# Optimization experiments

Hardware: AMD Instinct MI355X
Metric: run time of the kernel (lower is better)

The kernel has to match this reference:

```python
import jax, jax.numpy as jnp
import numpy as np

N, T, I, H = 16, 4096, 256, 512

def setup_inputs() -> dict:
    key = jax.random.key(0)
    k1, k2, k3, k4, k5 = jax.random.split(key, 5)
    x = jax.random.normal(k1, (N, T, I), dtype=jnp.float32)
    initial = jax.random.normal(k2, (N, H), dtype=jnp.float32)
    # nn.Linear params: y = x @ W.T + b
    Wi = jax.random.normal(k3, (H, I), dtype=jnp.float32) * (1.0 / np.sqrt(I))
    bi = jax.random.normal(k4, (H,), dtype=jnp.float32) * 0.01
    Whh = jax.random.normal(k5, (H, H), dtype=jnp.float32) * (1.0 / np.sqrt(H))
    return {"x": x, "initial": initial, "Wi": Wi, "bi": bi, "Whh": Whh}

def reference(x, initial, Wi, bi, Whh):
    # Precompute input projection for all timesteps: [N, T, H]
    proj = jnp.einsum('nti,hi->nth', x, Wi) + bi
    # h_0 = initial + Wi x[:,0]; h_t = Whh h_{t-1} + Wi x[:,t-1] for t >= 1
    h0 = initial + proj[:, 0]
    # inputs to scan: proj[:, 0:T-1] as [T-1, N, H] (note x[:,t-1] indexing)
    scan_in = jnp.swapaxes(proj[:, :T - 1], 0, 1)

    def step(h, p):
        h_new = h @ Whh.T + p
        return h_new, h_new

    _, ys = jax.lax.scan(step, h0, scan_in)  # ys: [T-1, N, H]
    hiddens = jnp.concatenate([h0[None], ys], axis=0)  # [T, N, H]
    hidden_tensor = jnp.swapaxes(hiddens, 0, 1)  # [N, T, H]
    return (hidden_tensor, hidden_tensor)
```

## Files before the change

kernel.cpp:

```cpp
#include <hip/hip_runtime.h>


constexpr int NN = 16;
constexpr int TT = 4096;
constexpr int II = 256;
constexpr int HH = 512;
constexpr int CK = 16;
constexpr int NC = 256;
constexpr long NTH = (long)NN * TT * HH;
constexpr int NMATS = 11;

__device__ __forceinline__ float4 ld4(const float* p) { return *(const float4*)p; }

#define FMA16(W_, e0, e1, e2, e3) \
    acc0.x = fmaf(e0, (W_).x, acc0.x); acc0.y = fmaf(e0, (W_).y, acc0.y); \
    acc0.z = fmaf(e0, (W_).z, acc0.z); acc0.w = fmaf(e0, (W_).w, acc0.w); \
    acc1.x = fmaf(e1, (W_).x, acc1.x); acc1.y = fmaf(e1, (W_).y, acc1.y); \
    acc1.z = fmaf(e1, (W_).z, acc1.z); acc1.w = fmaf(e1, (W_).w, acc1.w); \
    acc2.x = fmaf(e2, (W_).x, acc2.x); acc2.y = fmaf(e2, (W_).y, acc2.y); \
    acc2.z = fmaf(e2, (W_).z, acc2.z); acc2.w = fmaf(e2, (W_).w, acc2.w); \
    acc3.x = fmaf(e3, (W_).x, acc3.x); acc3.y = fmaf(e3, (W_).y, acc3.y); \
    acc3.z = fmaf(e3, (W_).z, acc3.z); acc3.w = fmaf(e3, (W_).w, acc3.w);

#define COMPUTE(sl) \
    FMA16(wv##sl[0], hv##sl[0].x, hv##sl[1].x, hv##sl[2].x, hv##sl[3].x) \
    FMA16(wv##sl[1], hv##sl[0].y, hv##sl[1].y, hv##sl[2].y, hv##sl[3].y) \
    FMA16(wv##sl[2], hv##sl[0].z, hv##sl[1].z, hv##sl[2].z, hv##sl[3].z) \
    FMA16(wv##sl[3], hv##sl[0].w, hv##sl[1].w, hv##sl[2].w, hv##sl[3].w)

#define PRE_PH(sl, kk) { \
    const float* wp_ = WT + (size_t)(4 * (kk)) * HH + j; \
    wv##sl[0] = ld4(wp_);            wv##sl[1] = ld4(wp_ + HH); \
    wv##sl[2] = ld4(wp_ + 2 * HH);   wv##sl[3] = ld4(wp_ + 3 * HH); \
    hv##sl[0] = hs[hb0 + (((kk)) ^ sw0)]; hv##sl[1] = hs[hb1 + (((kk)) ^ sw0)]; \
    hv##sl[2] = hs[hb2 + (((kk)) ^ sw1)]; hv##sl[3] = hs[hb3 + (((kk)) ^ sw1)]; }

#define PIPE_DECL float4 wv0[4], wv1[4], wv2[4], wv3[4]; \
                  float4 hv0[4], hv1[4], hv2[4], hv3[4];

__global__ __launch_bounds__(256) void trg_kernel(
    const float* __restrict__ src, float* __restrict__ dst, int R, int C)
{
    __shared__ float tile[32][33];
    const size_t mo = (size_t)blockIdx.z * R * C;
    const int x0 = blockIdx.x * 32, y0 = blockIdx.y * 32;
    const int tx = threadIdx.x & 31, ty = threadIdx.x >> 5;
#pragma unroll
    for (int r = 0; r < 4; r++)
        tile[ty + 8 * r][tx] = src[mo + (size_t)(y0 + ty + 8 * r) * C + (x0 + tx)];
    __syncthreads();
#pragma unroll
    for (int r = 0; r < 4; r++)
        dst[mo + (size_t)(x0 + ty + 8 * r) * R + (y0 + tx)] = tile[tx][ty + 8 * r];
}

__global__ __launch_bounds__(256) void proj_kernel(
    const float* __restrict__ x, const float* __restrict__ WiT,
    const float* __restrict__ bi, float* __restrict__ Bh)
{
    const int t0 = blockIdx.x * 32;
    const int j0 = blockIdx.y * 128;
    const int n  = blockIdx.z;
    __shared__ float4 xs[32 * 64];

    {
        const int r  = threadIdx.x >> 3;
        const int ci = threadIdx.x & 7;
        int s = t0 + r - 1; if (s < 0) s = 0;
        const float4* src = (const float4*)(x + ((size_t)n * TT + s) * II);
        const int rb = r * 64, rs = r >> 2;
#pragma unroll
        for (int q = 0; q < 8; q++) xs[rb + ((ci + 8 * q) ^ rs)] = src[ci + 8 * q];
    }
    __syncthreads();

    const int tj  = threadIdx.x & 31;
    const int tt4 = threadIdx.x >> 5;
    const int j   = j0 + tj * 4;
    const int xb0 = (tt4 * 4 + 0) * 64, xb1 = (tt4 * 4 + 1) * 64;
    const int xb2 = (tt4 * 4 + 2) * 64, xb3 = (tt4 * 4 + 3) * 64;
    const int swx = tt4;

    float4 acc0 = {0,0,0,0}, acc1 = {0,0,0,0}, acc2 = {0,0,0,0}, acc3 = {0,0,0,0};
    PIPE_DECL
#define PRE_PJ(sl, kk) { \
    const float* wp_ = WiT + (size_t)(4 * (kk)) * HH + j; \
    wv##sl[0] = ld4(wp_);            wv##sl[1] = ld4(wp_ + HH); \
    wv##sl[2] = ld4(wp_ + 2 * HH);   wv##sl[3] = ld4(wp_ + 3 * HH); \
    hv##sl[0] = xs[xb0 + (((kk)) ^ swx)]; hv##sl[1] = xs[xb1 + (((kk)) ^ swx)]; \
    hv##sl[2] = xs[xb2 + (((kk)) ^ swx)]; hv##sl[3] = xs[xb3 + (((kk)) ^ swx)]; }

    PRE_PJ(0, 0) PRE_PJ(1, 1) PRE_PJ(2, 2) PRE_PJ(3, 3)
    for (int g = 0; g < 15; g++) {
        const int kq = g * 4;
        COMPUTE(0) PRE_PJ(0, kq + 4)
        COMPUTE(1) PRE_PJ(1, kq + 5)
        COMPUTE(2) PRE_PJ(2, kq + 6)
        COMPUTE(3) PRE_PJ(3, kq + 7)
    }
    COMPUTE(0) COMPUTE(1) COMPUTE(2) COMPUTE(3)

    const float4 bv = ld4(bi + j);
    {
        const int tb = t0 + tt4 * 4;
        *(float4*)(Bh + ((size_t)n * TT + tb + 0) * HH + j) =
            make_float4(acc0.x + bv.x, acc0.y + bv.y, acc0.z + bv.z, acc0.w + bv.w);
        *(float4*)(Bh + ((size_t)n * TT + tb + 1) * HH + j) =
            make_float4(acc1.x + bv.x, acc1.y + bv.y, acc1.z + bv.z, acc1.w + bv.w);
        *(float4*)(Bh + ((size_t)n * TT + tb + 2) * HH + j) =
            make_float4(acc2.x + bv.x, acc2.y + bv.y, acc2.z + bv.z, acc2.w + bv.w);
        *(float4*)(Bh + ((size_t)n * TT + tb + 3) * HH + j) =
            make_float4(acc3.x + bv.x, acc3.y + bv.y, acc3.z + bv.z, acc3.w + bv.w);
    }
}

template <int PHASE>
__global__ __launch_bounds__(512, 2) void phase_kernel(
    const float* __restrict__ WT,
    float* __restrict__ Bh,
    const float* __restrict__ init_,
    const float* __restrict__ Gin,
    float* __restrict__ Zout,
    float* __restrict__ outA)
{
    __shared__ float4 hs[NN * 128];
    const int c   = blockIdx.x;
    const int tid = threadIdx.x;
    const int nq  = tid & 3;
    const int n0  = nq * 4;
    const int jq  = tid >> 2;
    const int j   = jq * 4;
    const int hb0 = (n0 + 0) * 128, hb1 = (n0 + 1) * 128;
    const int hb2 = (n0 + 2) * 128, hb3 = (n0 + 3) * 128;
    const int sw0 = nq * 2, sw1 = nq * 2 + 1;

    {
        float4 v[4];
        if (c == 0) {
#pragma unroll
            for (int rr = 0; rr < 4; rr++) {
                const int nn = n0 + rr;
                float4 iv = ld4(init_ + (size_t)nn * HH + j);
                float4 bv = ld4(Bh + (size_t)nn * TT * HH + j);
                v[rr] = make_float4(iv.x + bv.x, iv.y + bv.y, iv.z + bv.z, iv.w + bv.w);
                if (PHASE == 3) {
                    *(float4*)(outA + (size_t)nn * TT * HH + j) = v[rr];
                    *(float4*)(Bh   + (size_t)nn * TT * HH + j) = v[rr];
                }
            }
        } else if (PHASE == 1) {
            const int t0 = c * CK;
#pragma unroll
            for (int rr = 0; rr < 4; rr++)
                v[rr] = ld4(Bh + ((size_t)(n0 + rr) * TT + t0) * HH + j);
        } else {
#pragma unroll
            for (int rr = 0; rr < 4; rr++)
                v[rr] = ld4(Gin + (size_t)(c - 1) * NN * HH + (size_t)(n0 + rr) * HH + j);
        }
        hs[hb0 + (jq ^ sw0)] = v[0];
        hs[hb1 + (jq ^ sw0)] = v[1];
        hs[hb2 + (jq ^ sw1)] = v[2];
        hs[hb3 + (jq ^ sw1)] = v[3];
    }
    __syncthreads();

    const int tstart = (PHASE == 1) ? (c * CK + 1) : ((c == 0) ? 1 : c * CK);
    const int tend   = c * CK + CK;

    for (int t = tstart; t < tend; t++) {
        float* bp0 = Bh + ((size_t)(n0 + 0) * TT + t) * HH + j;
        float* bp1 = Bh + ((size_t)(n0 + 1) * TT + t) * HH + j;
        float* bp2 = Bh + ((size_t)(n0 + 2) * TT + t) * HH + j;
        float* bp3 = Bh + ((size_t)(n0 + 3) * TT + t) * HH + j;
        float4 b0 = ld4(bp0), b1 = ld4(bp1), b2 = ld4(bp2), b3 = ld4(bp3);

        float4 acc0 = {0,0,0,0}, acc1 = {0,0,0,0}, acc2 = {0,0,0,0}, acc3 = {0,0,0,0};
        PIPE_DECL
        PRE_PH(0, 0) PRE_PH(1, 1) PRE_PH(2, 2) PRE_PH(3, 3)
        for (int g = 0; g < 31; g++) {
            const int kq = g * 4;
            COMPUTE(0) PRE_PH(0, kq + 4)
            COMPUTE(1) PRE_PH(1, kq + 5)
            COMPUTE(2) PRE_PH(2, kq + 6)
            COMPUTE(3) PRE_PH(3, kq + 7)
        }
        COMPUTE(0) COMPUTE(1) COMPUTE(2) COMPUTE(3)

        float4 o0 = make_float4(acc0.x + b0.x, acc0.y + b0.y, acc0.z + b0.z, acc0.w + b0.w);
        float4 o1 = make_float4(acc1.x + b1.x, acc1.y + b1.y, acc1.z + b1.z, acc1.w + b1.w);
        float4 o2 = make_float4(acc2.x + b2.x, acc2.y + b2.y, acc2.z + b2.z, acc2.w + b2.w);
        float4 o3 = make_float4(acc3.x + b3.x, acc3.y + b3.y, acc3.z + b3.z, acc3.w + b3.w);

        __syncthreads();
        hs[hb0 + (jq ^ sw0)] = o0;
        hs[hb1 + (jq ^ sw0)] = o1;
        hs[hb2 + (jq ^ sw1)] = o2;
        hs[hb3 + (jq ^ sw1)] = o3;
        if (PHASE == 3) {
            *(float4*)(outA + ((size_t)(n0 + 0) * TT + t) * HH + j) = o0;
            *(float4*)(outA + ((size_t)(n0 + 1) * TT + t) * HH + j) = o1;
            *(float4*)(outA + ((size_t)(n0 + 2) * TT + t) * HH + j) = o2;
            *(float4*)(outA + ((size_t)(n0 + 3) * TT + t) * HH + j) = o3;
            *(float4*)bp0 = o0; *(float4*)bp1 = o1;
            *(float4*)bp2 = o2; *(float4*)bp3 = o3;
        }
        __syncthreads();
    }

    if (PHASE == 1) {
        float* zp = Zout + (size_t)c * NN * HH;
        *(float4*)(zp + (size_t)(n0 + 0) * HH + j) = hs[hb0 + (jq ^ sw0)];
        *(float4*)(zp + (size_t)(n0 + 1) * HH + j) = hs[hb1 + (jq ^ sw0)];
        *(float4*)(zp + (size_t)(n0 + 2) * HH + j) = hs[hb2 + (jq ^ sw1)];
        *(float4*)(zp + (size_t)(n0 + 3) * HH + j) = hs[hb3 + (jq ^ sw1)];
    }
}

__global__ __launch_bounds__(256) void sq_kernel(
    const float* __restrict__ A, float* __restrict__ Out)
{
    const int j0 = blockIdx.x * 128;
    const int a0 = blockIdx.y * 16;
    __shared__ float4 As[16 * 128];
    {
#pragma unroll
        for (int rr = 0; rr < 8; rr++) {
            int idx = threadIdx.x + rr * 256;
            int row = idx >> 7, s = idx & 127;
            As[row * 128 + (s ^ (row >> 2))] = ld4(A + (size_t)(a0 + row) * HH + s * 4);
        }
    }
    __syncthreads();

    const int jh = threadIdx.x & 63;
    const int j  = j0 + jh * 2;
    const int rq = threadIdx.x >> 6;
    const int ab0 = (rq * 4 + 0) * 128, ab1 = (rq * 4 + 1) * 128;
    const int ab2 = (rq * 4 + 2) * 128, ab3 = (rq * 4 + 3) * 128;

    float2 bw0[4], bw1[4], bw2[4], bw3[4];
    float4 av0[4], av1[4], av2[4], av3[4];
    float2 c0 = {0,0}, c1 = {0,0}, c2 = {0,0}, c3 = {0,0};
#define SQ_PRE(sl, kk) { \
    const float* bp_ = A + (size_t)(4 * (kk)) * HH + j; \
    bw##sl[0] = *(const float2*)(bp_);            bw##sl[1] = *(const float2*)(bp_ + HH); \
    bw##sl[2] = *(const float2*)(bp_ + 2 * HH);   bw##sl[3] = *(const float2*)(bp_ + 3 * HH); \
    av##sl[0] = As[ab0 + (((kk)) ^ rq)]; av##sl[1] = As[ab1 + (((kk)) ^ rq)]; \
    av##sl[2] = As[ab2 + (((kk)) ^ rq)]; av##sl[3] = As[ab3 + (((kk)) ^ rq)]; }
#define SQ_F(Bv_, e0, e1, e2, e3) \
    c0.x = fmaf(e0, (Bv_).x, c0.x); c0.y = fmaf(e0, (Bv_).y, c0.y); \
    c1.x = fmaf(e1, (Bv_).x, c1.x); c1.y = fmaf(e1, (Bv_).y, c1.y); \
    c2.x = fmaf(e2, (Bv_).x, c2.x); c2.y = fmaf(e2, (Bv_).y, c2.y); \
    c3.x = fmaf(e3, (Bv_).x, c3.x); c3.y = fmaf(e3, (Bv_).y, c3.y);
#define SQ_C(sl) \
    SQ_F(bw##sl[0], av##sl[0].x, av##sl[1].x, av##sl[2].x, av##sl[3].x) \
    SQ_F(bw##sl[1], av##sl[0].y, av##sl[1].y, av##sl[2].y, av##sl[3].y) \
    SQ_F(bw##sl[2], av##sl[0].z, av##sl[1].z, av##sl[2].z, av##sl[3].z) \
    SQ_F(bw##sl[3], av##sl[0].w, av##sl[1].w, av##sl[2].w, av##sl[3].w)

    SQ_PRE(0, 0) SQ_PRE(1, 1) SQ_PRE(2, 2) SQ_PRE(3, 3)
    for (int g = 0; g < 31; g++) {
        const int kq = g * 4;
        SQ_C(0) SQ_PRE(0, kq + 4)
        SQ_C(1) SQ_PRE(1, kq + 5)
        SQ_C(2) SQ_PRE(2, kq + 6)
        SQ_C(3) SQ_PRE(3, kq + 7)
    }
    SQ_C(0) SQ_C(1) SQ_C(2) SQ_C(3)

    *(float2*)(Out + (size_t)(a0 + rq * 4 + 0) * HH + j) = c0;
    *(float2*)(Out + (size_t)(a0 + rq * 4 + 1) * HH + j) = c1;
    *(float2*)(Out + (size_t)(a0 + rq * 4 + 2) * HH + j) = c2;
    *(float2*)(Out + (size_t)(a0 + rq * 4 + 3) * HH + j) = c3;
}

__global__ __launch_bounds__(512, 2) void ks_kernel(
    const float* __restrict__ Gin, float* __restrict__ Gout,
    const float* __restrict__ WT, int sft)
{
    __shared__ float4 hs[NN * 128];
    const int c   = blockIdx.x;
    const int tid = threadIdx.x;

    if (c < sft) {
        const float4* src = (const float4*)(Gin + (size_t)c * NN * HH);
        float4* dst = (float4*)(Gout + (size_t)c * NN * HH);
#pragma unroll
        for (int r = 0; r < 4; r++) dst[tid + r * 512] = src[tid + r * 512];
        return;
    }

    const int nq  = tid & 3;
    const int n0  = nq * 4;
    const int jq  = tid >> 2;
    const int j   = jq * 4;
    const int hb0 = (n0 + 0) * 128, hb1 = (n0 + 1) * 128;
    const int hb2 = (n0 + 2) * 128, hb3 = (n0 + 3) * 128;
    const int sw0 = nq * 2, sw1 = nq * 2 + 1;

    float4 g[4];
    {
        const float* sp = Gin + (size_t)(c - sft) * NN * HH;
        const float* gp = Gin + (size_t)c * NN * HH;
        float4 v[4];
#pragma unroll
        for (int rr = 0; rr < 4; rr++) {
            v[rr] = ld4(sp + (size_t)(n0 + rr) * HH + j);
            g[rr] = ld4(gp + (size_t)(n0 + rr) * HH + j);
        }
        hs[hb0 + (jq ^ sw0)] = v[0];
        hs[hb1 + (jq ^ sw0)] = v[1];
        hs[hb2 + (jq ^ sw1)] = v[2];
        hs[hb3 + (jq ^ sw1)] = v[3];
    }
    __syncthreads();

    float4 acc0 = {0,0,0,0}, acc1 = {0,0,0,0}, acc2 = {0,0,0,0}, acc3 = {0,0,0,0};
    PIPE_DECL
    PRE_PH(0, 0) PRE_PH(1, 1) PRE_PH(2, 2) PRE_PH(3, 3)
    for (int g2 = 0; g2 < 31; g2++) {
        const int kq = g2 * 4;
        COMPUTE(0) PRE_PH(0, kq + 4)
        COMPUTE(1) PRE_PH(1, kq + 5)
        COMPUTE(2) PRE_PH(2, kq + 6)
        COMPUTE(3) PRE_PH(3, kq + 7)
    }
    COMPUTE(0) COMPUTE(1) COMPUTE(2) COMPUTE(3)

    float* op = Gout + (size_t)c * NN * HH;
    *(float4*)(op + (size_t)(n0 + 0) * HH + j) =
        make_float4(g[0].x + acc0.x, g[0].y + acc0.y, g[0].z + acc0.z, g[0].w + acc0.w);
    *(float4*)(op + (size_t)(n0 + 1) * HH + j) =
        make_float4(g[1].x + acc1.x, g[1].y + acc1.y, g[1].z + acc1.z, g[1].w + acc1.w);
    *(float4*)(op + (size_t)(n0 + 2) * HH + j) =
        make_float4(g[2].x + acc2.x, g[2].y + acc2.y, g[2].z + acc2.z, g[2].w + acc2.w);
    *(float4*)(op + (size_t)(n0 + 3) * HH + j) =
        make_float4(g[3].x + acc3.x, g[3].y + acc3.y, g[3].z + acc3.z, g[3].w + acc3.w);
}

extern "C" void kernel_launch(void* const* d_in, const int* in_sizes, int n_in,
                              void* d_out, int out_size, void* d_ws, size_t ws_size,
                              hipStream_t stream)
{
    const float* x    = (const float*)d_in[0];
    const float* ini  = (const float*)d_in[1];
    const float* Wi   = (const float*)d_in[2];
    const float* bi   = (const float*)d_in[3];
    const float* Whh  = (const float*)d_in[4];
    float* out   = (float*)d_out;
    float* halfB = out + NTH;
    float* mats  = out + NTH - (long)NMATS * HH * HH;
    float* matsT = out + NTH - (long)(NMATS + 8) * HH * HH;
    float* WiT   = matsT - (long)II * HH;
    float* G0 = (float*)d_ws;
    float* G1 = G0 + (size_t)NC * NN * HH;

    trg_kernel<<<dim3(II / 32, HH / 32, 1), 256, 0, stream>>>(Wi, WiT, HH, II);
    proj_kernel<<<dim3(TT / 32, HH / 128, NN), 256, 0, stream>>>(x, WiT, bi, halfB);

    trg_kernel<<<dim3(16, 16, 1), 256, 0, stream>>>(Whh, G1, HH, HH);

    phase_kernel<1><<<dim3(NC), 512, 0, stream>>>(G1, halfB, ini, nullptr, G0, nullptr);

    sq_kernel<<<dim3(4, 32), 256, 0, stream>>>(Whh, mats);
    for (int i = 1; i < NMATS; i++)
        sq_kernel<<<dim3(4, 32), 256, 0, stream>>>(mats + (size_t)(i - 1) * HH * HH,
                                                   mats + (size_t)i * HH * HH);
    trg_kernel<<<dim3(16, 16, 8), 256, 0, stream>>>(mats + (size_t)3 * HH * HH, matsT,
                                                    HH, HH);

    for (int r = 0; r < 8; r++) {
        const float* src = (r & 1) ? G1 : G0;
        float* dst       = (r & 1) ? G0 : G1;
        ks_kernel<<<dim3(NC), 512, 0, stream>>>(src, dst,
                                                matsT + (size_t)r * HH * HH, 1 << r);
    }

    trg_kernel<<<dim3(16, 16, 1), 256, 0, stream>>>(Whh, G1, HH, HH);

    phase_kernel<3><<<dim3(NC), 512, 0, stream>>>(G1, halfB, ini, G0, nullptr, out);
}
```

Before: 2.129 ms.

## Halve chunk length to 512 chunks, add scan round, hoist weight preloads

Halves the chunk length to 8 timesteps and doubles the chunk count to 512. This shortens the serial per-chunk recurrence in both phase kernels, at the cost of one extra Kogge-Stone round using an additional matrix power. The first W prefetch moves out of the timestep loop and is re-issued at the tail of each step, and per-step pointer recomputation becomes pointer increments. Buffers are re-laid out: the carry buffer lives partly in the output tail, and the transposed Whh is computed once and reused instead of being transposed twice.

```diff
diff --git a/kernel.cpp b/kernel.cpp
--- a/kernel.cpp
+++ b/kernel.cpp
@@ -5,10 +5,11 @@
 constexpr int TT = 4096;
 constexpr int II = 256;
 constexpr int HH = 512;
-constexpr int CK = 16;
-constexpr int NC = 256;
+constexpr int CK = 8;
+constexpr int NC = 512;
 constexpr long NTH = (long)NN * TT * HH;
 constexpr int NMATS = 11;
+constexpr int NKS = 9;
 
 __device__ __forceinline__ float4 ld4(const float* p) { return *(const float4*)p; }
 
@@ -28,12 +29,14 @@
     FMA16(wv##sl[2], hv##sl[0].z, hv##sl[1].z, hv##sl[2].z, hv##sl[3].z) \
     FMA16(wv##sl[3], hv##sl[0].w, hv##sl[1].w, hv##sl[2].w, hv##sl[3].w)
 
-#define PRE_PH(sl, kk) { \
+#define PRE_W(sl, kk) { \
     const float* wp_ = WT + (size_t)(4 * (kk)) * HH + j; \
     wv##sl[0] = ld4(wp_);            wv##sl[1] = ld4(wp_ + HH); \
-    wv##sl[2] = ld4(wp_ + 2 * HH);   wv##sl[3] = ld4(wp_ + 3 * HH); \
+    wv##sl[2] = ld4(wp_ + 2 * HH);   wv##sl[3] = ld4(wp_ + 3 * HH); }
+#define PRE_H(sl, kk) { \
     hv##sl[0] = hs[hb0 + (((kk)) ^ sw0)]; hv##sl[1] = hs[hb1 + (((kk)) ^ sw0)]; \
     hv##sl[2] = hs[hb2 + (((kk)) ^ sw1)]; hv##sl[3] = hs[hb3 + (((kk)) ^ sw1)]; }
+#define PRE_PH(sl, kk) { PRE_W(sl, kk) PRE_H(sl, kk) }
 
 #define PIPE_DECL float4 wv0[4], wv1[4], wv2[4], wv3[4]; \
                   float4 hv0[4], hv1[4], hv2[4], hv3[4];
@@ -168,16 +171,23 @@
     const int tstart = (PHASE == 1) ? (c * CK + 1) : ((c == 0) ? 1 : c * CK);
     const int tend   = c * CK + CK;
 
+    float* bp0 = Bh + ((size_t)(n0 + 0) * TT + tstart) * HH + j;
+    float* bp1 = Bh + ((size_t)(n0 + 1) * TT + tstart) * HH + j;
+    float* bp2 = Bh + ((size_t)(n0 + 2) * TT + tstart) * HH + j;
+    float* bp3 = Bh + ((size_t)(n0 + 3) * TT + tstart) * HH + j;
+    float* op0 = outA + ((size_t)(n0 + 0) * TT + tstart) * HH + j;
+    float* op1 = outA + ((size_t)(n0 + 1) * TT + tstart) * HH + j;
+    float* op2 = outA + ((size_t)(n0 + 2) * TT + tstart) * HH + j;
+    float* op3 = outA + ((size_t)(n0 + 3) * TT + tstart) * HH + j;
+
+    PIPE_DECL
+    PRE_W(0, 0) PRE_W(1, 1) PRE_W(2, 2) PRE_W(3, 3)
+
     for (int t = tstart; t < tend; t++) {
-        float* bp0 = Bh + ((size_t)(n0 + 0) * TT + t) * HH + j;
-        float* bp1 = Bh + ((size_t)(n0 + 1) * TT + t) * HH + j;
-        float* bp2 = Bh + ((size_t)(n0 + 2) * TT + t) * HH + j;
-        float* bp3 = Bh + ((size_t)(n0 + 3) * TT + t) * HH + j;
         float4 b0 = ld4(bp0), b1 = ld4(bp1), b2 = ld4(bp2), b3 = ld4(bp3);
 
         float4 acc0 = {0,0,0,0}, acc1 = {0,0,0,0}, acc2 = {0,0,0,0}, acc3 = {0,0,0,0};
-        PIPE_DECL
-        PRE_PH(0, 0) PRE_PH(1, 1) PRE_PH(2, 2) PRE_PH(3, 3)
+        PRE_H(0, 0) PRE_H(1, 1) PRE_H(2, 2) PRE_H(3, 3)
         for (int g = 0; g < 31; g++) {
             const int kq = g * 4;
             COMPUTE(0) PRE_PH(0, kq + 4)
@@ -185,7 +195,10 @@
             COMPUTE(2) PRE_PH(2, kq + 6)
             COMPUTE(3) PRE_PH(3, kq + 7)
         }
-        COMPUTE(0) COMPUTE(1) COMPUTE(2) COMPUTE(3)
+        COMPUTE(0) PRE_W(0, 0)
+        COMPUTE(1) PRE_W(1, 1)
+        COMPUTE(2) PRE_W(2, 2)
+        COMPUTE(3) PRE_W(3, 3)
 
         float4 o0 = make_float4(acc0.x + b0.x, acc0.y + b0.y, acc0.z + b0.z, acc0.w + b0.w);
         float4 o1 = make_float4(acc1.x + b1.x, acc1.y + b1.y, acc1.z + b1.z, acc1.w + b1.w);
@@ -198,13 +211,13 @@
         hs[hb2 + (jq ^ sw1)] = o2;
         hs[hb3 + (jq ^ sw1)] = o3;
         if (PHASE == 3) {
-            *(float4*)(outA + ((size_t)(n0 + 0) * TT + t) * HH + j) = o0;
-            *(float4*)(outA + ((size_t)(n0 + 1) * TT + t) * HH + j) = o1;
-            *(float4*)(outA + ((size_t)(n0 + 2) * TT + t) * HH + j) = o2;
-            *(float4*)(outA + ((size_t)(n0 + 3) * TT + t) * HH + j) = o3;
+            *(float4*)op0 = o0; *(float4*)op1 = o1;
+            *(float4*)op2 = o2; *(float4*)op3 = o3;
             *(float4*)bp0 = o0; *(float4*)bp1 = o1;
             *(float4*)bp2 = o2; *(float4*)bp3 = o3;
-        }
+            op0 += HH; op1 += HH; op2 += HH; op3 += HH;
+        }
+        bp0 += HH; bp1 += HH; bp2 += HH; bp3 += HH;
         __syncthreads();
     }
 
@@ -350,34 +363,35 @@
     const float* Whh  = (const float*)d_in[4];
     float* out   = (float*)d_out;
     float* halfB = out + NTH;
+
     float* mats  = out + NTH - (long)NMATS * HH * HH;
-    float* matsT = out + NTH - (long)(NMATS + 8) * HH * HH;
+    float* matsT = mats - (long)NKS * HH * HH;
     float* WiT   = matsT - (long)II * HH;
-    float* G0 = (float*)d_ws;
-    float* G1 = G0 + (size_t)NC * NN * HH;
+    float* tailG = WiT - (long)NC * NN * HH;
+
+    float* wsG  = (float*)d_ws;
+    float* wsWT = wsG + (size_t)NC * NN * HH;
 
     trg_kernel<<<dim3(II / 32, HH / 32, 1), 256, 0, stream>>>(Wi, WiT, HH, II);
+    trg_kernel<<<dim3(16, 16, 1), 256, 0, stream>>>(Whh, wsWT, HH, HH);
+
     proj_kernel<<<dim3(TT / 32, HH / 128, NN), 256, 0, stream>>>(x, WiT, bi, halfB);
 
-    trg_kernel<<<dim3(16, 16, 1), 256, 0, stream>>>(Whh, G1, HH, HH);
-
-    phase_kernel<1><<<dim3(NC), 512, 0, stream>>>(G1, halfB, ini, nullptr, G0, nullptr);
+    phase_kernel<1><<<dim3(NC), 512, 0, stream>>>(wsWT, halfB, ini, nullptr, tailG, nullptr);
 
     sq_kernel<<<dim3(4, 32), 256, 0, stream>>>(Whh, mats);
     for (int i = 1; i < NMATS; i++)
         sq_kernel<<<dim3(4, 32), 256, 0, stream>>>(mats + (size_t)(i - 1) * HH * HH,
                                                    mats + (size_t)i * HH * HH);
-    trg_kernel<<<dim3(16, 16, 8), 256, 0, stream>>>(mats + (size_t)3 * HH * HH, matsT,
-                                                    HH, HH);
-
-    for (int r = 0; r < 8; r++) {
-        const float* src = (r & 1) ? G1 : G0;
-        float* dst       = (r & 1) ? G0 : G1;
+    trg_kernel<<<dim3(16, 16, NKS), 256, 0, stream>>>(mats + (size_t)2 * HH * HH, matsT,
+                                                      HH, HH);
+
+    for (int r = 0; r < NKS; r++) {
+        const float* src = (r & 1) ? wsG : tailG;
+        float* dst       = (r & 1) ? tailG : wsG;
         ks_kernel<<<dim3(NC), 512, 0, stream>>>(src, dst,
                                                 matsT + (size_t)r * HH * HH, 1 << r);
     }
 
-    trg_kernel<<<dim3(16, 16, 1), 256, 0, stream>>>(Whh, G1, HH, HH);
-
-    phase_kernel<3><<<dim3(NC), 512, 0, stream>>>(G1, halfB, ini, G0, nullptr, out);
-}
+    phase_kernel<3><<<dim3(NC), 512, 0, stream>>>(wsWT, halfB, ini, wsG, nullptr, out);
+}
```

New measurement: 2.715 ms. 27.5% more time.
